# Kernel tuning notes

Hardware: AMD Instinct MI355X
Metric: run time of the kernel (lower is better)

The kernel has to match this reference:

```python
import jax, jax.numpy as jnp
import numpy as np

EPS = 1e-06
N_HEADS = 8


def setup_inputs() -> dict:
    key = jax.random.key(0)
    ks = jax.random.split(key, 9)
    B, M, T, C = 2, 64, 256, 512
    s = 0.02
    return {
        "x": jax.random.normal(ks[0], (B, M, T, C), dtype=jnp.float32),
        "Wq": jax.random.normal(ks[1], (C, C), dtype=jnp.float32) * s,
        "bq": jnp.zeros((C,), dtype=jnp.float32),
        "Wk": jax.random.normal(ks[2], (C, C), dtype=jnp.float32) * s,
        "bk": jnp.zeros((C,), dtype=jnp.float32),
        "Wv": jax.random.normal(ks[3], (C, C), dtype=jnp.float32) * s,
        "bv": jnp.zeros((C,), dtype=jnp.float32),
        "Wp": jax.random.normal(ks[4], (C, C), dtype=jnp.float32) * s,
        "bp": jnp.zeros((C,), dtype=jnp.float32),
    }


def _proj_heads(x, W, b, N, D):
    # nn.Linear: x @ W.T + b, then view(B,M,T,N,D).transpose(2,3) -> [B,M,N,T,D]
    B, M, T, C = x.shape
    y = jnp.einsum('bmtc,dc->bmtd', x, W) + b
    return y.reshape(B, M, T, N, D).transpose(0, 1, 3, 2, 4)


def reference(x, Wq, bq, Wk, bk, Wv, bv, Wp, bp):
    B, M, T, C = x.shape
    N = N_HEADS
    D = C // N
    q = _proj_heads(x, Wq, bq, N, D)  # [B,M,N,T,D]
    k = _proj_heads(x, Wk, bk, N, D)
    v = _proj_heads(x, Wv, bv, N, D)
    # ELU+1 feature map
    q = jax.nn.elu(q) + 1.0
    k = jax.nn.elu(k) + 1.0
    # KtV = k^T @ v : [B,M,N,D,D]
    KtV = jnp.einsum('bmntd,bmnte->bmnde', k, v)
    # Z = 1 / (q @ sum_t k + eps) : [B,M,N,T]
    ksum = jnp.sum(k, axis=-2)  # [B,M,N,D]
    z = 1.0 / (jnp.einsum('bmntd,bmnd->bmnt', q, ksum) + EPS)
    # Original does Z.expand(...,D) @ KtV; since Z is constant over the D axis,
    # this equals z[t] * sum_d KtV[d, e] -- compute that directly (faithful math).
    KtV_colsum = jnp.sum(KtV, axis=-2)  # [B,M,N,D]
    V = z[..., None] * KtV_colsum[..., None, :]  # [B,M,N,T,D]
    V = V.transpose(0, 1, 3, 2, 4).reshape(B, M, T, N * D)
    out = jnp.einsum('bmtc,dc->bmtd', V, Wp) + bp
    return out
```

## Files before the change

kernel.cpp:

```cpp
#include <hip/hip_runtime.h>
#include <hip/hip_bf16.h>

#define BM_ 128
#define T_  256
#define C_  512
#define NH  8
#define DH  64

typedef __bf16 bf16;
typedef __attribute__((ext_vector_type(8))) __bf16 bf16x8;
typedef __attribute__((ext_vector_type(4))) float f32x4;

__device__ __forceinline__ float elu1(float v){ return v > 0.f ? v + 1.f : __expf(v); }

__device__ __forceinline__ unsigned short f2bf(float f){
  unsigned u = __float_as_uint(f);
  u += 0x7fffu + ((u >> 16) & 1u);
  return (unsigned short)(u >> 16);
}

__device__ __forceinline__ float bf2f(unsigned short b){
  return __uint_as_float(((unsigned)b) << 16);
}

#define GLOAD16(gptr, lptr) __builtin_amdgcn_global_load_lds( \
  (const __attribute__((address_space(1))) void*)(gptr), \
  (__attribute__((address_space(3))) void*)(lptr), 16, 0, 0)

#define FENCE() asm volatile("" ::: "memory")

__global__ __launch_bounds__(256) void cvt3_kernel(
    const float* __restrict__ a, int na4,
    const float* __restrict__ b, int nb4,
    const float* __restrict__ c, int nc4,
    unsigned short* __restrict__ oa, unsigned short* __restrict__ ob,
    unsigned short* __restrict__ oc)
{
  int i = blockIdx.x * blockDim.x + threadIdx.x;
  int stride = gridDim.x * blockDim.x;
  int total = na4 + nb4 + nc4;
  for (; i < total; i += stride) {
    const float* src; unsigned short* dst; int idx;
    if (i < na4)            { src = a; dst = oa; idx = i; }
    else if (i < na4 + nb4) { src = b; dst = ob; idx = i - na4; }
    else                    { src = c; dst = oc; idx = i - na4 - nb4; }
    float4 v = reinterpret_cast<const float4*>(src)[idx];
    ushort4 o;
    o.x = f2bf(v.x); o.y = f2bf(v.y); o.z = f2bf(v.z); o.w = f2bf(v.w);
    reinterpret_cast<ushort4*>(dst)[idx] = o;
  }
}

template<int MODE>
__global__ __launch_bounds__(512, 4) void gemm_proj(
    const bf16* __restrict__ A, const bf16* __restrict__ Bw,
    const float* __restrict__ bias,
    float* __restrict__ krow, float* __restrict__ ksum4,
    const float* __restrict__ ksum4_in, float* __restrict__ zden)
{
  __shared__ bf16 As[2][256 * 32];
  __shared__ bf16 Bs[2][128 * 32];

  const int tid  = threadIdx.x;
  const int lane = tid & 63;
  const int wid  = tid >> 6;
  const int wr   = wid >> 1, wc = wid & 1;

  const int L  = ((blockIdx.x & 7) << 6) + (blockIdx.x >> 3);
  const int tn = L & 3, tm = L >> 2;

  const bf16* Ab = A  + (size_t)(tm * 256) * C_;
  const bf16* Bb = Bw + (size_t)(tn * 128) * C_;
  const int fr = lane & 15, fq = lane >> 4;

  f32x4 acc[4][4];
#pragma unroll
  for (int m = 0; m < 4; ++m)
#pragma unroll
    for (int n = 0; n < 4; ++n) acc[m][n] = (f32x4){0.f, 0.f, 0.f, 0.f};

#define SW(r, s) ((s) ^ (((r) ^ ((r) >> 2)) & 3))
#define LOFF(row, sl) ((row) * 32 + (SW(row, sl) << 3))

#define STGA(b, kt) do { \
  _Pragma("unroll") \
  for (int j = 0; j < 2; ++j) { \
    int d_ = j * 512 + tid; int r_ = d_ >> 2; int s_ = d_ & 3; \
    GLOAD16(Ab + (size_t)r_ * C_ + (kt) * 32 + (SW(r_, s_) << 3), \
            &As[b][d_ * 8]); \
  } } while (0)

#define STGB(b, kt) do { \
    int r_ = tid >> 2; int s_ = tid & 3; \
    GLOAD16(Bb + (size_t)r_ * C_ + (kt) * 32 + (SW(r_, s_) << 3), \
            &Bs[b][tid * 8]); \
  } while (0)

  STGA(0, 0); STGB(0, 0);
  asm volatile("s_waitcnt vmcnt(0)" ::: "memory");
  __builtin_amdgcn_s_barrier();
  FENCE();

  bf16x8 af[4], bfr[4];

  for (int t = 0; t < 16; ++t) {
    const int cur = t & 1;
#pragma unroll
    for (int m = 0; m < 4; ++m)
      af[m] = *reinterpret_cast<const bf16x8*>(&As[cur][LOFF(wr * 64 + m * 16 + fr, fq)]);
#pragma unroll
    for (int n = 0; n < 4; ++n)
      bfr[n] = *reinterpret_cast<const bf16x8*>(&Bs[cur][LOFF(wc * 64 + n * 16 + fr, fq)]);
    if (t < 15) { STGA(cur ^ 1, t + 1); STGB(cur ^ 1, t + 1); }
    __builtin_amdgcn_s_setprio(1);
#pragma unroll
    for (int m = 0; m < 4; ++m)
#pragma unroll
      for (int n = 0; n < 4; ++n)
        acc[m][n] = __builtin_amdgcn_mfma_f32_16x16x32_bf16(af[m], bfr[n], acc[m][n], 0, 0, 0);
    __builtin_amdgcn_s_setprio(0);
    if (t < 15) {
      asm volatile("s_waitcnt vmcnt(0)" ::: "memory");
      __builtin_amdgcn_s_barrier();
      FENCE();
    }
  }
#undef STGA
#undef STGB
#undef LOFF
#undef SW

  const int bm   = tm;
  const int head = tn * 2 + wc;
  float bj[4];
#pragma unroll
  for (int n = 0; n < 4; ++n) bj[n] = bias[tn * 128 + wc * 64 + n * 16 + fr];

  if (MODE == 0) {
    float cs[4] = {0.f, 0.f, 0.f, 0.f};
#pragma unroll
    for (int m = 0; m < 4; ++m) {
#pragma unroll
      for (int r = 0; r < 4; ++r) {
        float rs = 0.f;
#pragma unroll
        for (int n = 0; n < 4; ++n) {
          float v = elu1(acc[m][n][r] + bj[n]);
          rs += v;
          cs[n] += v;
        }
#pragma unroll
        for (int msk = 1; msk < 16; msk <<= 1) rs += __shfl_xor(rs, msk);
        if (fr == 0) {
          int tg = wr * 64 + m * 16 + fq * 4 + r;
          krow[((size_t)bm * NH + head) * T_ + tg] = rs;
        }
      }
    }
#pragma unroll
    for (int n = 0; n < 4; ++n) {
      cs[n] += __shfl_xor(cs[n], 16);
      cs[n] += __shfl_xor(cs[n], 32);
      if (fq == 0)
        ksum4[((size_t)wr * BM_ + bm) * C_ + tn * 128 + wc * 64 + n * 16 + fr] = cs[n];
    }
  } else {
    float ks[4];
#pragma unroll
    for (int n = 0; n < 4; ++n) {
      size_t col = (size_t)bm * C_ + tn * 128 + wc * 64 + n * 16 + fr;
      ks[n] = ksum4_in[col] + ksum4_in[(size_t)BM_ * C_ + col]
            + ksum4_in[2 * (size_t)BM_ * C_ + col] + ksum4_in[3 * (size_t)BM_ * C_ + col];
    }
#pragma unroll
    for (int m = 0; m < 4; ++m) {
#pragma unroll
      for (int r = 0; r < 4; ++r) {
        float zs = 0.f;
#pragma unroll
        for (int n = 0; n < 4; ++n) zs = fmaf(elu1(acc[m][n][r] + bj[n]), ks[n], zs);
#pragma unroll
        for (int msk = 1; msk < 16; msk <<= 1) zs += __shfl_xor(zs, msk);
        if (fr == 0) {
          int tg = wr * 64 + m * 16 + fq * 4 + r;
          zden[((size_t)bm * NH + head) * T_ + tg] = zs;
        }
      }
    }
  }
}

__global__ __launch_bounds__(256) void xk_kernel(
    const unsigned short* __restrict__ xb, const float* __restrict__ krow,
    float* __restrict__ xk4, float* __restrict__ srow4)
{
  const int bm = blockIdx.x, qt = blockIdx.y, tid = threadIdx.x;
  __shared__ float krs[NH * 64];
#pragma unroll
  for (int p = 0; p < 2; ++p) {
    int idx = tid + p * 256;
    int n = idx >> 6, t = idx & 63;
    krs[idx] = krow[((size_t)bm * NH + n) * T_ + qt * 64 + t];
  }
  __syncthreads();
  float a0[8], a1[8];
#pragma unroll
  for (int n = 0; n < 8; ++n) { a0[n] = 0.f; a1[n] = 0.f; }
  const unsigned short* xp = xb + ((size_t)bm * T_ + qt * 64) * C_ + tid * 2;
  for (int t = 0; t < 64; ++t) {
    ushort2 u = *reinterpret_cast<const ushort2*>(xp + (size_t)t * C_);
    float x0 = bf2f(u.x), x1 = bf2f(u.y);
#pragma unroll
    for (int n = 0; n < 8; ++n) {
      float kr = krs[n * 64 + t];
      a0[n] = fmaf(kr, x0, a0[n]);
      a1[n] = fmaf(kr, x1, a1[n]);
    }
  }
#pragma unroll
  for (int n = 0; n < 8; ++n)
    *reinterpret_cast<float2*>(&xk4[(((size_t)qt * BM_ + bm) * NH + n) * C_ + tid * 2])
        = make_float2(a0[n], a1[n]);
  if (tid < 8) {
    float s = 0.f;
    for (int t = 0; t < 64; ++t) s += krs[tid * 64 + t];
    srow4[((size_t)qt * BM_ + bm) * NH + tid] = s;
  }
}

__global__ __launch_bounds__(256) void colsum_kernel(
    const float* __restrict__ xk4, const float* __restrict__ srow4,
    const float* __restrict__ Wv, const float* __restrict__ bv,
    float* __restrict__ cs_g)
{
  const int bm0 = blockIdx.x * 8, h = blockIdx.y, tid = threadIdx.x;
  __shared__ float4 xs4[8][128];
#pragma unroll
  for (int p = 0; p < 4; ++p) {
    int idx = tid + p * 256;
    int bmr = idx >> 7, c4 = idx & 127;
    float4 s = make_float4(0.f, 0.f, 0.f, 0.f);
#pragma unroll
    for (int q = 0; q < 4; ++q) {
      float4 u = *reinterpret_cast<const float4*>(
          xk4 + (((size_t)q * BM_ + bm0 + bmr) * NH + h) * C_ + c4 * 4);
      s.x += u.x; s.y += u.y; s.z += u.z; s.w += u.w;
    }
    xs4[bmr][c4] = s;
  }
  __syncthreads();
  const int e = tid & 63, bs = tid >> 6;
  const float4* wv4 = reinterpret_cast<const float4*>(Wv + (size_t)(h * DH + e) * C_);
  float acc0 = 0.f, acc1 = 0.f;
#pragma unroll 4
  for (int c4 = 0; c4 < 128; ++c4) {
    float4 w = wv4[c4];
    float4 a = xs4[bs * 2][c4];
    float4 b = xs4[bs * 2 + 1][c4];
    acc0 += w.x * a.x + w.y * a.y + w.z * a.z + w.w * a.w;
    acc1 += w.x * b.x + w.y * b.y + w.z * b.z + w.w * b.w;
  }
  float bve = bv[h * DH + e];
  int bmA = bm0 + bs * 2, bmB = bmA + 1;
  float sA = 0.f, sB = 0.f;
#pragma unroll
  for (int q = 0; q < 4; ++q) {
    sA += srow4[((size_t)q * BM_ + bmA) * NH + h];
    sB += srow4[((size_t)q * BM_ + bmB) * NH + h];
  }
  cs_g[((size_t)bmA * NH + h) * DH + e] = acc0 + sA * bve;
  cs_g[((size_t)bmB * NH + h) * DH + e] = acc1 + sB * bve;
}

__global__ __launch_bounds__(256) void wbuf_kernel(
    const float* __restrict__ cs_g, const float* __restrict__ Wp,
    float* __restrict__ wbuf)
{
  const int cpt = blockIdx.x, h = blockIdx.y, bm0 = blockIdx.z * 16;
  const int tid = threadIdx.x;
  __shared__ float4 csL4[16][16];
  {
    int bmr = tid >> 4, e4 = tid & 15;
    csL4[bmr][e4] = *reinterpret_cast<const float4*>(
        cs_g + ((size_t)(bm0 + bmr) * NH + h) * DH + e4 * 4);
  }
  __syncthreads();
  const int cp = cpt * 256 + tid;
  float4 wp[16];
  const float4* wpr = reinterpret_cast<const float4*>(Wp + (size_t)cp * C_ + h * DH);
#pragma unroll
  for (int e4 = 0; e4 < 16; ++e4) wp[e4] = wpr[e4];
#pragma unroll
  for (int bmr = 0; bmr < 16; ++bmr) {
    float acc = 0.f;
#pragma unroll
    for (int e4 = 0; e4 < 16; ++e4) {
      float4 c = csL4[bmr][e4];
      acc += wp[e4].x * c.x + wp[e4].y * c.y + wp[e4].z * c.z + wp[e4].w * c.w;
    }
    wbuf[((size_t)(bm0 + bmr) * NH + h) * C_ + cp] = acc;
  }
}

__global__ __launch_bounds__(256) void out_kernel(
    const float* __restrict__ zden, const float* __restrict__ wbuf,
    const float* __restrict__ bp, float* __restrict__ out)
{
  const int bm = blockIdx.x, tt = blockIdx.y, tid = threadIdx.x;
  __shared__ float zs[NH][64];
#pragma unroll
  for (int p = 0; p < 2; ++p) {
    int idx = tid + p * 256;
    int n = idx >> 6, t = idx & 63;
    zs[n][t] = 1.f / (zden[((size_t)bm * NH + n) * T_ + tt * 64 + t] + 1e-6f);
  }
  float2 wv[8];
  const int c2 = tid * 2;
#pragma unroll
  for (int n = 0; n < 8; ++n)
    wv[n] = *reinterpret_cast<const float2*>(wbuf + ((size_t)bm * NH + n) * C_ + c2);
  float2 bpv = *reinterpret_cast<const float2*>(bp + c2);
  __syncthreads();
  float* ob = out + ((size_t)bm * T_ + tt * 64) * C_;
  for (int t = 0; t < 64; ++t) {
    float o0 = bpv.x, o1 = bpv.y;
#pragma unroll
    for (int n = 0; n < 8; ++n) { float z = zs[n][t]; o0 = fmaf(z, wv[n].x, o0); o1 = fmaf(z, wv[n].y, o1); }
    *reinterpret_cast<float2*>(ob + (size_t)t * C_ + c2) = make_float2(o0, o1);
  }
}

extern "C" void kernel_launch(void* const* d_in, const int* in_sizes, int n_in,
                              void* d_out, int out_size, void* d_ws, size_t ws_size,
                              hipStream_t stream)
{
  const float* x  = (const float*)d_in[0];
  const float* Wq = (const float*)d_in[1];
  const float* bq = (const float*)d_in[2];
  const float* Wk = (const float*)d_in[3];
  const float* bk = (const float*)d_in[4];
  const float* Wv = (const float*)d_in[5];
  const float* bv = (const float*)d_in[6];
  const float* Wp = (const float*)d_in[7];
  const float* bp = (const float*)d_in[8];
  float* out = (float*)d_out;

  float* ws    = (float*)d_ws;
  float* zden  = ws;
  float* ksum4 = zden + 262144;
  float* krow  = ksum4 + 262144;
  float* srow4 = krow + 262144;
  float* xk4   = srow4 + 4096;
  float* cs    = xk4 + 2097152;
  float* wbuf  = cs + 65536;
  unsigned short* xb  = (unsigned short*)(wbuf + 524288);
  unsigned short* wkb = xb + 16777216;
  unsigned short* wqb = wkb + 262144;

  cvt3_kernel<<<2048, 256, 0, stream>>>(x, 16777216 / 4, Wk, 262144 / 4, Wq, 262144 / 4,
                                        xb, wkb, wqb);

  gemm_proj<0><<<512, 512, 0, stream>>>((const bf16*)xb, (const bf16*)wkb, bk,
                                        krow, ksum4, nullptr, nullptr);
  xk_kernel<<<dim3(BM_, 4), 256, 0, stream>>>(xb, krow, xk4, srow4);
  colsum_kernel<<<dim3(16, 8), 256, 0, stream>>>(xk4, srow4, Wv, bv, cs);
  wbuf_kernel<<<dim3(2, 8, 8), 256, 0, stream>>>(cs, Wp, wbuf);
  gemm_proj<1><<<512, 512, 0, stream>>>((const bf16*)xb, (const bf16*)wqb, bq,
                                        nullptr, ksum4, ksum4, zden);
  out_kernel<<<dim3(BM_, 4), 256, 0, stream>>>(zden, wbuf, bp, out);
}
```

Baseline: 116.6 us.

## Retile projection GEMM to 128x256 with B fragments read directly from global

Changes the projection GEMM block tile from 256x128 to 128x256 with a 2x4 wave layout and a 64-wide K step. B (weight) fragments are now loaded straight from global/L2 into registers instead of being staged through LDS, which halves LDS use and removes the B staging. The aim is to cut LDS traffic and the number of barriers, at the cost of uncoalesced, latency-exposed global loads for B and more register pressure. The epilogue indexing is adjusted so the ksum partial sums still fill four slots.

```diff
diff --git a/kernel.cpp b/kernel.cpp
--- a/kernel.cpp
+++ b/kernel.cpp
@@ -58,83 +58,85 @@
     float* __restrict__ krow, float* __restrict__ ksum4,
     const float* __restrict__ ksum4_in, float* __restrict__ zden)
 {
-  __shared__ bf16 As[2][256 * 32];
-  __shared__ bf16 Bs[2][128 * 32];
+  __shared__ bf16 As[2][128 * 64];
 
   const int tid  = threadIdx.x;
   const int lane = tid & 63;
   const int wid  = tid >> 6;
-  const int wr   = wid >> 1, wc = wid & 1;
-
-  const int L  = ((blockIdx.x & 7) << 6) + (blockIdx.x >> 3);
-  const int tn = L & 3, tm = L >> 2;
-
-  const bf16* Ab = A  + (size_t)(tm * 256) * C_;
-  const bf16* Bb = Bw + (size_t)(tn * 128) * C_;
+  const int wr   = wid >> 2, wc = wid & 3;
+
+  const int L  = (blockIdx.x & 7) * 64 + (blockIdx.x >> 3);
+  const int tn = L & 1, tm = L >> 1;
+
+  const bf16* Ab = A  + (size_t)(tm * 128) * C_;
   const int fr = lane & 15, fq = lane >> 4;
 
+  const bf16* Bl = Bw + (size_t)(tn * 256 + wc * 64 + fr) * C_ + fq * 8;
+
   f32x4 acc[4][4];
 #pragma unroll
   for (int m = 0; m < 4; ++m)
 #pragma unroll
     for (int n = 0; n < 4; ++n) acc[m][n] = (f32x4){0.f, 0.f, 0.f, 0.f};
 
-#define SW(r, s) ((s) ^ (((r) ^ ((r) >> 2)) & 3))
-#define LOFF(row, sl) ((row) * 32 + (SW(row, sl) << 3))
-
-#define STGA(b, kt) do { \
+#define STG(b, kt) do { \
   _Pragma("unroll") \
   for (int j = 0; j < 2; ++j) { \
-    int d_ = j * 512 + tid; int r_ = d_ >> 2; int s_ = d_ & 3; \
-    GLOAD16(Ab + (size_t)r_ * C_ + (kt) * 32 + (SW(r_, s_) << 3), \
+    int d_ = j * 512 + tid; int r_ = d_ >> 3; int s_ = d_ & 7; \
+    GLOAD16(Ab + (size_t)r_ * C_ + (kt) * 64 + ((s_ ^ (r_ & 7)) << 3), \
             &As[b][d_ * 8]); \
   } } while (0)
 
-#define STGB(b, kt) do { \
-    int r_ = tid >> 2; int s_ = tid & 3; \
-    GLOAD16(Bb + (size_t)r_ * C_ + (kt) * 32 + (SW(r_, s_) << 3), \
-            &Bs[b][tid * 8]); \
-  } while (0)
-
-  STGA(0, 0); STGB(0, 0);
+  STG(0, 0);
   asm volatile("s_waitcnt vmcnt(0)" ::: "memory");
   __builtin_amdgcn_s_barrier();
   FENCE();
 
-  bf16x8 af[4], bfr[4];
-
-  for (int t = 0; t < 16; ++t) {
+  for (int t = 0; t < 8; ++t) {
     const int cur = t & 1;
-#pragma unroll
-    for (int m = 0; m < 4; ++m)
-      af[m] = *reinterpret_cast<const bf16x8*>(&As[cur][LOFF(wr * 64 + m * 16 + fr, fq)]);
-#pragma unroll
-    for (int n = 0; n < 4; ++n)
-      bfr[n] = *reinterpret_cast<const bf16x8*>(&Bs[cur][LOFF(wc * 64 + n * 16 + fr, fq)]);
-    if (t < 15) { STGA(cur ^ 1, t + 1); STGB(cur ^ 1, t + 1); }
-    __builtin_amdgcn_s_setprio(1);
-#pragma unroll
-    for (int m = 0; m < 4; ++m)
+
+    bf16x8 bfr[8];
+#pragma unroll
+    for (int kk = 0; kk < 2; ++kk)
 #pragma unroll
       for (int n = 0; n < 4; ++n)
-        acc[m][n] = __builtin_amdgcn_mfma_f32_16x16x32_bf16(af[m], bfr[n], acc[m][n], 0, 0, 0);
-    __builtin_amdgcn_s_setprio(0);
-    if (t < 15) {
+        bfr[kk * 4 + n] = *reinterpret_cast<const bf16x8*>(
+            Bl + (size_t)n * 16 * C_ + t * 64 + kk * 32);
+
+    if (t < 7) STG(cur ^ 1, t + 1);
+
+#pragma unroll
+    for (int kk = 0; kk < 2; ++kk) {
+      bf16x8 af[4];
+#pragma unroll
+      for (int m = 0; m < 4; ++m) {
+        int row = wr * 64 + m * 16 + fr;
+        af[m] = *reinterpret_cast<const bf16x8*>(
+            &As[cur][row * 64 + (((kk * 4 + fq) ^ (fr & 7)) << 3)]);
+      }
+      __builtin_amdgcn_s_setprio(1);
+#pragma unroll
+      for (int m = 0; m < 4; ++m)
+#pragma unroll
+        for (int n = 0; n < 4; ++n)
+          acc[m][n] = __builtin_amdgcn_mfma_f32_16x16x32_bf16(af[m], bfr[kk * 4 + n], acc[m][n], 0, 0, 0);
+      __builtin_amdgcn_s_setprio(0);
+    }
+
+    if (t < 7) {
       asm volatile("s_waitcnt vmcnt(0)" ::: "memory");
       __builtin_amdgcn_s_barrier();
       FENCE();
     }
   }
-#undef STGA
-#undef STGB
-#undef LOFF
-#undef SW
-
-  const int bm   = tm;
-  const int head = tn * 2 + wc;
+#undef STG
+
+  const int bm    = tm >> 1;
+  const int thalf = tm & 1;
+  const int head  = tn * 4 + wc;
   float bj[4];
 #pragma unroll
-  for (int n = 0; n < 4; ++n) bj[n] = bias[tn * 128 + wc * 64 + n * 16 + fr];
+  for (int n = 0; n < 4; ++n) bj[n] = bias[tn * 256 + wc * 64 + n * 16 + fr];
 
   if (MODE == 0) {
     float cs[4] = {0.f, 0.f, 0.f, 0.f};
@@ -152,23 +154,24 @@
 #pragma unroll
         for (int msk = 1; msk < 16; msk <<= 1) rs += __shfl_xor(rs, msk);
         if (fr == 0) {
-          int tg = wr * 64 + m * 16 + fq * 4 + r;
+          int tg = thalf * 128 + wr * 64 + m * 16 + fq * 4 + r;
           krow[((size_t)bm * NH + head) * T_ + tg] = rs;
         }
       }
     }
+    const int part = thalf * 2 + wr;
 #pragma unroll
     for (int n = 0; n < 4; ++n) {
       cs[n] += __shfl_xor(cs[n], 16);
       cs[n] += __shfl_xor(cs[n], 32);
       if (fq == 0)
-        ksum4[((size_t)wr * BM_ + bm) * C_ + tn * 128 + wc * 64 + n * 16 + fr] = cs[n];
+        ksum4[((size_t)part * BM_ + bm) * C_ + tn * 256 + wc * 64 + n * 16 + fr] = cs[n];
     }
   } else {
     float ks[4];
 #pragma unroll
     for (int n = 0; n < 4; ++n) {
-      size_t col = (size_t)bm * C_ + tn * 128 + wc * 64 + n * 16 + fr;
+      size_t col = (size_t)bm * C_ + tn * 256 + wc * 64 + n * 16 + fr;
       ks[n] = ksum4_in[col] + ksum4_in[(size_t)BM_ * C_ + col]
             + ksum4_in[2 * (size_t)BM_ * C_ + col] + ksum4_in[3 * (size_t)BM_ * C_ + col];
     }
@@ -182,7 +185,7 @@
 #pragma unroll
         for (int msk = 1; msk < 16; msk <<= 1) zs += __shfl_xor(zs, msk);
         if (fr == 0) {
-          int tg = wr * 64 + m * 16 + fq * 4 + r;
+          int tg = thalf * 128 + wr * 64 + m * 16 + fq * 4 + r;
           zden[((size_t)bm * NH + head) * T_ + tg] = zs;
         }
       }
```

After: 149.5 us. 28.2% more time.
